# Optimization experiments

Hardware: AMD Instinct MI355X
Metric: run time of the kernel (lower is better)

## Reference

```python
import jax, jax.numpy as jnp
import numpy as np

B, L, D = 4, 8192, 512


def _normalize(v):
    # F.normalize: v / max(||v||, 1e-12)
    n = jnp.linalg.norm(v, axis=-1, keepdims=True)
    return v / jnp.maximum(n, 1e-12)


def setup_inputs() -> dict:
    key = jax.random.key(0)
    k1, k2, k3, k4 = jax.random.split(key, 4)
    return {
        "hidden_states": jax.random.normal(k1, (B, L, D), jnp.float32),
        "residual": jax.random.normal(k2, (B, L, D), jnp.float32),
        "q_weight": jax.random.normal(k3, (D, D), jnp.float32) * 0.02,
        "k_weight": jax.random.normal(k4, (D, D), jnp.float32) * 0.02,
        "det_state": jnp.zeros((B, D), jnp.float32),
    }


def reference(hidden_states, residual, q_weight, k_weight, det_state):
    Bs, Ls, Ds = hidden_states.shape
    # ---- CosineSimRouter.prob_boundary ----
    q = _normalize(hidden_states[:, :-1] @ q_weight.T)   # (B, L-1, D)
    k = _normalize(hidden_states[:, 1:] @ k_weight.T)    # (B, L-1, D)
    cos_sim = jnp.einsum('bld,bld->bl', q, k)            # (B, L-1)
    prob = jnp.concatenate(
        [jnp.ones((Bs, 1), jnp.float32), jnp.clip((1.0 - cos_sim) / 2.0, 0.0, 1.0)],
        axis=1)                                           # (B, L); prob[:,0]=1 (state=None path)
    token_mask = prob > 0.5                               # (B, L)

    # ---- Tokenizer: compact boundary positions (pad M -> L, static shape) ----
    counts = token_mask.sum(axis=1)                       # (B,)
    order = jnp.argsort(~token_mask, axis=1)              # stable: True-mask indices first, in order
    valid = jnp.arange(Ls)[None, :] < counts[:, None]     # (B, L)
    chunked = jnp.take_along_axis(hidden_states, order[..., None], axis=1)
    chunked = chunked * valid[..., None]                  # (B, L, D)
    chunk_probs = jnp.take_along_axis(prob, order, axis=1) * valid  # (B, L)

    # ---- DeTokenizer: EMA associative scan over compacted chunks ----
    decay = jnp.clip(1.0 - chunk_probs, 0.0, 1.0)
    # pad positions have chunk_probs=0 -> decay=1 -> state carried unchanged
    a = jnp.broadcast_to(decay[..., None], (Bs, Ls, Ds))
    b = (1.0 - decay)[..., None] * chunked
    b = b.at[:, 0].add(a[:, 0] * det_state)

    def comb(x, y):  # x earlier, y later: (a2*a1, a2*b1 + b2)
        ax, bx = x
        ay, by = y
        return ax * ay, ay * bx + by

    _, ema_out = jax.lax.associative_scan(comb, (a, b), axis=1)
    ema_out = ema_out * valid[..., None]                  # zero padded chunk slots

    # broadcast back to full sequence via cumulative chunk indexing
    chunk_idx = jnp.cumsum(token_mask.astype(jnp.int32), axis=1) - 1  # (B, L)
    ci = jnp.clip(chunk_idx, 0, Ls - 1)
    long_states = jnp.take_along_axis(ema_out, ci[..., None], axis=1)
    long_states = long_states * (chunk_idx >= 0)[..., None]

    # STE coefficient: forward == 1 (grad flows through max(1-p, p) in bwd)
    coef_raw = jnp.maximum(1.0 - prob, prob)
    coef = coef_raw + jax.lax.stop_gradient(1.0 - coef_raw)
    long_states = long_states * coef[..., None]

    output = residual + long_states                       # (B, L, D)
    return output
```

## Files before the change

### kernel.cpp

```cpp
#include <hip/hip_runtime.h>
#include <hip/hip_bf16.h>
#include <math.h>

#define B_  4
#define L_  8192
#define D_  512

#define BM   128
#define NCT  4
#define NRT  (L_ / BM)
#define KW   64
#define NSTAGE (D_ / KW)

#define CHUNK 64
#define NCHUNK (L_ / CHUNK)

#define MAXFIX 16380
#define FIX_TAU 1.0e-3f
#define FROWS 8
#define NSLICE 8

typedef short bf16x8 __attribute__((ext_vector_type(8)));
typedef float f32x4 __attribute__((ext_vector_type(4)));
typedef unsigned short u16;
typedef unsigned int u32;

__device__ __forceinline__ u32 pk2(float lo, float hi) {
    __hip_bfloat162 v = __float22bfloat162_rn(float2{lo, hi});
    union { __hip_bfloat162 b; u32 u; } cv; cv.b = v;
    return cv.u;
}

#define GLOAD_LDS(g, l) __builtin_amdgcn_global_load_lds( \
    (__attribute__((address_space(1))) void*)(g),         \
    (__attribute__((address_space(3))) void*)(l), 16, 0, 0)

__global__ __launch_bounds__(256) void conv_h(
    const float* __restrict__ h, u16* __restrict__ h16)
{
    size_t i = ((size_t)blockIdx.x * 256 + threadIdx.x) * 8;
    float4 a = *(const float4*)(h + i);
    float4 b = *(const float4*)(h + i + 4);
    uint4 v;
    v.x = pk2(a.x, a.y); v.y = pk2(a.z, a.w);
    v.z = pk2(b.x, b.y); v.w = pk2(b.z, b.w);
    *(uint4*)(h16 + i) = v;
}

__global__ __launch_bounds__(256) void prep_w(
    const float* __restrict__ wq, const float* __restrict__ wk,
    u16* __restrict__ qh, u16* __restrict__ kh,
    float* __restrict__ wqt, float* __restrict__ wkt,
    int* __restrict__ fix_cnt)
{
    __shared__ float tile[64][65];
    const int bi = blockIdx.x;
    const int bj = blockIdx.y;
    const int t = threadIdx.x;
    if (bi == 0 && bj == 0 && t == 0) *fix_cnt = 0;
    const int c0 = bi * 64, k0 = bj * 64;
    const float* src = wq; float* dst = wqt; u16* dsth = qh;
#pragma unroll
    for (int m = 0; m < 2; ++m) {
        __syncthreads();
#pragma unroll
        for (int it = 0; it < 4; ++it) {
            int r = it * 16 + (t >> 4);
            int cc = (t & 15) * 4;
            float4 v = *(const float4*)(src + (size_t)(c0 + r) * D_ + k0 + cc);
            tile[r][cc] = v.x; tile[r][cc + 1] = v.y;
            tile[r][cc + 2] = v.z; tile[r][cc + 3] = v.w;
            uint2 hv; hv.x = pk2(v.x, v.y); hv.y = pk2(v.z, v.w);
            *(uint2*)(dsth + (size_t)(c0 + r) * D_ + k0 + cc) = hv;
        }
        __syncthreads();
#pragma unroll
        for (int it = 0; it < 4; ++it) {
            int cl = t & 63;
            int kq = it * 4 + (t >> 6);
            float4 v;
            v.x = tile[cl][kq * 4 + 0]; v.y = tile[cl][kq * 4 + 1];
            v.z = tile[cl][kq * 4 + 2]; v.w = tile[cl][kq * 4 + 3];
            size_t o = ((size_t)((k0 >> 2) + kq) * 512 + (c0 + cl)) * 4;
            *(float4*)(dst + o) = v;
        }
        src = wk; dst = wkt; dsth = kh;
    }
}

__global__ __launch_bounds__(256, 2) void qk_mfma(
    const u16* __restrict__ h16,
    const u16* __restrict__ wqh, const u16* __restrict__ wkh,
    float* __restrict__ part)
{
    const int bid = blockIdx.x;
    const int swz = (bid & 7) * 128 + (bid >> 3);
    const int ct = swz & 3, rt = (swz >> 2) & 63, b = swz >> 8;
    const int t = threadIdx.x, wid = t >> 6, lane = t & 63;
    const int l15 = lane & 15, l4 = lane >> 4;

    __shared__ __align__(16) u16 ah[2][129 * 64];
    __shared__ float red[4][BM][3];

    const int r0 = rt * BM;
    const u16* hb = h16 + (size_t)b * L_ * D_;

    const int rl0 = wid * 32 + (lane >> 3);
    const int csw = ((lane & 7) ^ (rl0 & 7)) * 8;
    const u16* gA = hb + (size_t)(r0 + rl0) * D_ + csw;
    const int dstw = wid * 32 * 64;

    const int re = (r0 + BM > L_ - 1) ? (L_ - 1) : (r0 + BM);
    const u16* gpe = hb + (size_t)re * D_;

    const int colb = ct * 128 + wid * 32;
    const u16* bq0 = wqh + (size_t)(colb + l15) * D_ + l4 * 8;
    const u16* bq1 = bq0 + (size_t)16 * D_;
    const u16* bk0 = wkh + (size_t)(colb + l15) * D_ + l4 * 8;
    const u16* bk1 = bk0 + (size_t)16 * D_;

    int aoff[8];
#pragma unroll
    for (int rf = 0; rf < 8; ++rf) {
        int R = rf * 16 + l15;
        aoff[rf] = R * 64 + ((l4 ^ (R & 7)) * 8);
    }
    const int aoffE = 128 * 64 + l4 * 8;

    f32x4 accq[8][2], acck[8][2], ackl[2];
    const f32x4 zero = {0.f, 0.f, 0.f, 0.f};
#pragma unroll
    for (int rf = 0; rf < 8; ++rf) {
        accq[rf][0] = zero; accq[rf][1] = zero;
        acck[rf][0] = zero; acck[rf][1] = zero;
    }
    ackl[0] = zero; ackl[1] = zero;

#define STAGE_ISSUE(S, BUF) do { const int _o = (S) * KW;      \
    GLOAD_LDS(gA + _o,         &ah[BUF][dstw]);                \
    GLOAD_LDS(gA + _o + 4096,  &ah[BUF][dstw + 512]);          \
    GLOAD_LDS(gA + _o + 8192,  &ah[BUF][dstw + 1024]);         \
    GLOAD_LDS(gA + _o + 12288, &ah[BUF][dstw + 1536]); } while (0)

    STAGE_ISSUE(0, 0);
    uint2 er = {0, 0};
    if (t < 16) er = *(const uint2*)(gpe + t * 4);
    if (t < 16) *(uint2*)(&ah[0][128 * 64 + t * 4]) = er;
    __syncthreads();

    int cur = 0;
    for (int s = 0; s < NSTAGE; ++s) {
        if (s + 1 < NSTAGE) {
            STAGE_ISSUE(s + 1, cur ^ 1);
            if (t < 16) er = *(const uint2*)(gpe + (s + 1) * KW + t * 4);
        }

        const int so = s * KW;
        bf16x8 q00 = *(const bf16x8*)(bq0 + so);
        bf16x8 q01 = *(const bf16x8*)(bq0 + so + 32);
        bf16x8 q10 = *(const bf16x8*)(bq1 + so);
        bf16x8 q11 = *(const bf16x8*)(bq1 + so + 32);
        bf16x8 k00 = *(const bf16x8*)(bk0 + so);
        bf16x8 k01 = *(const bf16x8*)(bk0 + so + 32);
        bf16x8 k10 = *(const bf16x8*)(bk1 + so);
        bf16x8 k11 = *(const bf16x8*)(bk1 + so + 32);

        const u16* ab = ah[cur];
#pragma unroll
        for (int kk = 0; kk < 2; ++kk) {
            bf16x8 fq0 = kk ? q01 : q00;
            bf16x8 fq1 = kk ? q11 : q10;
            bf16x8 fk0 = kk ? k01 : k00;
            bf16x8 fk1 = kk ? k11 : k10;
#pragma unroll
            for (int rf = 0; rf < 8; ++rf) {
                bf16x8 a = *(const bf16x8*)(ab + (aoff[rf] ^ (kk * 32)));
                accq[rf][0] = __builtin_amdgcn_mfma_f32_16x16x32_bf16(a, fq0, accq[rf][0], 0, 0, 0);
                accq[rf][1] = __builtin_amdgcn_mfma_f32_16x16x32_bf16(a, fq1, accq[rf][1], 0, 0, 0);
                acck[rf][0] = __builtin_amdgcn_mfma_f32_16x16x32_bf16(a, fk0, acck[rf][0], 0, 0, 0);
                acck[rf][1] = __builtin_amdgcn_mfma_f32_16x16x32_bf16(a, fk1, acck[rf][1], 0, 0, 0);
            }
            bf16x8 al = *(const bf16x8*)(ab + (aoffE ^ (kk * 32)));
            ackl[0] = __builtin_amdgcn_mfma_f32_16x16x32_bf16(al, fk0, ackl[0], 0, 0, 0);
            ackl[1] = __builtin_amdgcn_mfma_f32_16x16x32_bf16(al, fk1, ackl[1], 0, 0, 0);
        }

        if (s + 1 < NSTAGE && t < 16)
            *(uint2*)(&ah[cur ^ 1][128 * 64 + t * 4]) = er;
        __syncthreads();
        cur ^= 1;
    }
#undef STAGE_ISSUE

#pragma unroll
    for (int rf = 0; rf < 8; ++rf) {
#pragma unroll
        for (int reg = 0; reg < 4; ++reg) {
            float pq = 0.f, pk = 0.f, pd = 0.f;
#pragma unroll
            for (int cf = 0; cf < 2; ++cf) {
                float qv = accq[rf][cf][reg];
                float kv = acck[rf][cf][reg];
                pq += qv * qv;
                pk += kv * kv;
                float ksh;
                if (reg < 3) {
                    ksh = acck[rf][cf][reg + 1];
                } else {
                    float up = __shfl(acck[rf][cf][0], (lane + 16) & 63);
                    float nx0 = (rf < 7) ? acck[rf + 1][cf][0] : ackl[cf][0];
                    float nx = __shfl(nx0, l15);
                    ksh = (l4 == 3) ? nx : up;
                }
                pd += qv * ksh;
            }
#pragma unroll
            for (int off = 1; off < 16; off <<= 1) {
                pq += __shfl_xor(pq, off);
                pk += __shfl_xor(pk, off);
                pd += __shfl_xor(pd, off);
            }
            if (l15 == 0) {
                int row = rf * 16 + l4 * 4 + reg;
                red[wid][row][0] = pq;
                red[wid][row][1] = pk;
                red[wid][row][2] = pd;
            }
        }
    }
    __syncthreads();
    if (t < BM) {
        float pq = red[0][t][0] + red[1][t][0] + red[2][t][0] + red[3][t][0];
        float pk = red[0][t][1] + red[1][t][1] + red[2][t][1] + red[3][t][1];
        float pd = red[0][t][2] + red[1][t][2] + red[2][t][2] + red[3][t][2];
        size_t o = (((size_t)ct * B_ + b) * L_ + (r0 + t)) * 3;
        part[o + 0] = pq; part[o + 1] = pk; part[o + 2] = pd;
    }
}

__global__ __launch_bounds__(256) void cos_reduce(
    const float* __restrict__ part, float* __restrict__ p,
    int* __restrict__ fix_cnt, int* __restrict__ fix_list)
{
    int idx = blockIdx.x * 256 + threadIdx.x;
    if (idx >= B_ * L_) return;
    int b = idx / L_;
    int tp = idx % L_;
    if (tp == 0) { p[idx] = 1.0f; return; }
    int l = tp - 1;
    float nq = 0.f, nk = 0.f, dt = 0.f;
#pragma unroll
    for (int ct = 0; ct < NCT; ++ct) {
        size_t o = (((size_t)ct * B_ + b) * L_ + l) * 3;
        nq += part[o + 0];
        dt += part[o + 2];
        nk += part[o + 4];
    }
    float qn = sqrtf(nq); if (qn < 1e-12f) qn = 1e-12f;
    float kn = sqrtf(nk); if (kn < 1e-12f) kn = 1e-12f;
    float cs = dt / (qn * kn);
    float pr = 0.5f * (1.0f - cs);
    pr = fminf(fmaxf(pr, 0.0f), 1.0f);
    p[idx] = pr;
    if (fabsf(cs) < FIX_TAU) {
        int slot = atomicAdd(fix_cnt, 1);
        if (slot < MAXFIX) fix_list[slot] = idx;
    }
}

__global__ __launch_bounds__(256) void fixup_main(
    const float* __restrict__ h,
    const float* __restrict__ wqt, const float* __restrict__ wkt,
    const int* __restrict__ fix_cnt, const int* __restrict__ fix_list,
    float* __restrict__ part_fix)
{
    __shared__ float hq[FROWS][D_];
    __shared__ float hk[FROWS][D_];
    __shared__ float red[FROWS][3][4];
    const int t = threadIdx.x, wid = t >> 6, lane = t & 63;
    const int col16 = lane & 15, kpart = lane >> 4;
    int n = *fix_cnt; if (n > MAXFIX) n = MAXFIX;
    const int ntiles = (n + FROWS - 1) / FROWS;
    const int nitems = ntiles * NSLICE;

    for (int item = blockIdx.x; item < nitems; item += gridDim.x) {
        const int tile = item >> 3;
        const int cs = item & 7;
        __syncthreads();
#pragma unroll
        for (int r = 0; r < FROWS; ++r) {
            int s = tile * FROWS + r;
            int idx = fix_list[s < n ? s : 0];
            int bb = idx >> 13;
            int tp = idx & (L_ - 1);
            const float* hr = h + ((size_t)bb * L_ + (tp - 1)) * D_;
            ((float2*)hq[r])[t] = ((const float2*)hr)[t];
            ((float2*)hk[r])[t] = ((const float2*)(hr + D_))[t];
        }
        __syncthreads();

        const int c = cs * 64 + wid * 16 + col16;
        float qa0, qa1, qa2, qa3, qa4, qa5, qa6, qa7;
        float ka0, ka1, ka2, ka3, ka4, ka5, ka6, ka7;
        qa0=qa1=qa2=qa3=qa4=qa5=qa6=qa7=0.f;
        ka0=ka1=ka2=ka3=ka4=ka5=ka6=ka7=0.f;

        const int k0 = kpart * 32;
        float4 wv = *(const float4*)(wqt + ((size_t)k0 * 512 + c) * 4);
        float4 xv = *(const float4*)(wkt + ((size_t)k0 * 512 + c) * 4);
#pragma unroll 4
        for (int kq = k0; kq < k0 + 32; ++kq) {
            const int kn = (kq + 1 < k0 + 32) ? kq + 1 : kq;
            float4 wn = *(const float4*)(wqt + ((size_t)kn * 512 + c) * 4);
            float4 xn = *(const float4*)(wkt + ((size_t)kn * 512 + c) * 4);
#define FROW(R, QA, KA) { \
            float4 hv = *(const float4*)(&hq[R][kq * 4]); \
            float4 kv = *(const float4*)(&hk[R][kq * 4]); \
            QA += hv.x*wv.x + hv.y*wv.y + hv.z*wv.z + hv.w*wv.w; \
            KA += kv.x*xv.x + kv.y*xv.y + kv.z*xv.z + kv.w*xv.w; }
            FROW(0, qa0, ka0) FROW(1, qa1, ka1) FROW(2, qa2, ka2) FROW(3, qa3, ka3)
            FROW(4, qa4, ka4) FROW(5, qa5, ka5) FROW(6, qa6, ka6) FROW(7, qa7, ka7)
#undef FROW
            wv = wn; xv = xn;
        }

#define REDROW(R, QA, KA) { \
        float qf = QA; qf += __shfl_xor(qf, 16); qf += __shfl_xor(qf, 32); \
        float kf = KA; kf += __shfl_xor(kf, 16); kf += __shfl_xor(kf, 32); \
        float pq = qf * qf, pk = kf * kf, pd = qf * kf; \
        pq += __shfl_xor(pq, 1); pk += __shfl_xor(pk, 1); pd += __shfl_xor(pd, 1); \
        pq += __shfl_xor(pq, 2); pk += __shfl_xor(pk, 2); pd += __shfl_xor(pd, 2); \
        pq += __shfl_xor(pq, 4); pk += __shfl_xor(pk, 4); pd += __shfl_xor(pd, 4); \
        pq += __shfl_xor(pq, 8); pk += __shfl_xor(pk, 8); pd += __shfl_xor(pd, 8); \
        if (lane == 0) { red[R][0][wid] = pq; red[R][1][wid] = pk; red[R][2][wid] = pd; } }
        REDROW(0, qa0, ka0) REDROW(1, qa1, ka1) REDROW(2, qa2, ka2) REDROW(3, qa3, ka3)
        REDROW(4, qa4, ka4) REDROW(5, qa5, ka5) REDROW(6, qa6, ka6) REDROW(7, qa7, ka7)
#undef REDROW
        __syncthreads();
        if (t < FROWS) {
            int s = tile * FROWS + t;
            if (s < n) {
                float* pp = part_fix + ((size_t)s * NSLICE + cs) * 3;
                pp[0] = red[t][0][0] + red[t][0][1] + red[t][0][2] + red[t][0][3];
                pp[1] = red[t][1][0] + red[t][1][1] + red[t][1][2] + red[t][1][3];
                pp[2] = red[t][2][0] + red[t][2][1] + red[t][2][2] + red[t][2][3];
            }
        }
    }
}

__global__ __launch_bounds__(256) void fixup_final(
    const int* __restrict__ fix_cnt, const int* __restrict__ fix_list,
    const float* __restrict__ part_fix, float* __restrict__ p)
{
    int n = *fix_cnt; if (n > MAXFIX) n = MAXFIX;
    for (int s = blockIdx.x * 256 + threadIdx.x; s < n; s += gridDim.x * 256) {
        float nq = 0.f, nk = 0.f, dt = 0.f;
#pragma unroll
        for (int cs = 0; cs < NSLICE; ++cs) {
            const float* pp = part_fix + ((size_t)s * NSLICE + cs) * 3;
            nq += pp[0]; nk += pp[1]; dt += pp[2];
        }
        float qn = sqrtf(nq); if (qn < 1e-12f) qn = 1e-12f;
        float kn = sqrtf(nk); if (kn < 1e-12f) kn = 1e-12f;
        float cs2 = dt / (qn * kn);
        float pr = 0.5f * (1.0f - cs2);
        pr = fminf(fmaxf(pr, 0.0f), 1.0f);
        p[fix_list[s]] = pr;
    }
}

__global__ __launch_bounds__(256) void scan_a(
    const float* __restrict__ h, const float* __restrict__ p,
    float* __restrict__ Bc, float* __restrict__ Ac)
{
    const int t = threadIdx.x;
    const int c = blockIdx.x, b = blockIdx.y;
    const int l0 = c * CHUNK;
    const float* pb = p + (size_t)b * L_ + l0;
    const float2* hb = (const float2*)(h + ((size_t)b * L_ + l0) * D_) + t;

    float2 st = {0.f, 0.f};
    float ap = 1.f;
#pragma unroll 4
    for (int i = 0; i < CHUNK; ++i) {
        float pr = pb[i];
        float2 hv = hb[(size_t)i * 256];
        bool sel = pr > 0.5f;
        float a = sel ? 1.f - pr : 1.f;
        float g = sel ? pr : 0.f;
        st.x = a * st.x + g * hv.x;
        st.y = a * st.y + g * hv.y;
        ap *= a;
    }
    ((float2*)Bc)[((size_t)b * NCHUNK + c) * 256 + t] = st;
    if (t == 0) Ac[b * NCHUNK + c] = ap;
}

__global__ __launch_bounds__(256) void scan_b(
    const float* __restrict__ Ac, const float* __restrict__ Bc,
    const float* __restrict__ det, float* __restrict__ carry)
{
    const int t = threadIdx.x;
    const int b = blockIdx.x;
    const float* acb = Ac + b * NCHUNK;
    const float2* bcb = (const float2*)Bc + (size_t)b * NCHUNK * 256 + t;
    float2* cb = (float2*)carry + (size_t)b * NCHUNK * 256 + t;
    float2 st = ((const float2*)det)[(size_t)b * 256 + t];

    float a0 = acb[0], a1 = acb[1], a2 = acb[2], a3 = acb[3];
    float2 b0 = bcb[0], b1 = bcb[256], b2 = bcb[512], b3 = bcb[768];
    for (int g = 0; g < NCHUNK / 4; ++g) {
        const int nc = (g + 1 < NCHUNK / 4) ? (g + 1) * 4 : g * 4;
        float an0 = acb[nc], an1 = acb[nc + 1], an2 = acb[nc + 2], an3 = acb[nc + 3];
        float2 bn0 = bcb[(size_t)nc * 256],        bn1 = bcb[(size_t)(nc + 1) * 256];
        float2 bn2 = bcb[(size_t)(nc + 2) * 256],  bn3 = bcb[(size_t)(nc + 3) * 256];
        const size_t c0 = (size_t)g * 4 * 256;
        cb[c0]       = st; st.x = a0 * st.x + b0.x; st.y = a0 * st.y + b0.y;
        cb[c0 + 256] = st; st.x = a1 * st.x + b1.x; st.y = a1 * st.y + b1.y;
        cb[c0 + 512] = st; st.x = a2 * st.x + b2.x; st.y = a2 * st.y + b2.y;
        cb[c0 + 768] = st; st.x = a3 * st.x + b3.x; st.y = a3 * st.y + b3.y;
        a0 = an0; a1 = an1; a2 = an2; a3 = an3;
        b0 = bn0; b1 = bn1; b2 = bn2; b3 = bn3;
    }
}

__global__ __launch_bounds__(256) void scan_c(
    const float* __restrict__ h, const float* __restrict__ p,
    const float* __restrict__ res, const float* __restrict__ carry,
    float* __restrict__ out)
{
    const int t = threadIdx.x;
    const int c = blockIdx.x, b = blockIdx.y;
    const int l0 = c * CHUNK;
    const float* pb = p + (size_t)b * L_ + l0;
    const size_t base = ((size_t)b * L_ + l0) * 256 + t;
    const float2* hb = (const float2*)h + base;
    const float2* rb = (const float2*)res + base;
    float2* ob = (float2*)out + base;

    float2 st = ((const float2*)carry)[((size_t)b * NCHUNK + c) * 256 + t];
#pragma unroll 4
    for (int i = 0; i < CHUNK; ++i) {
        float pr = pb[i];
        float2 hv = hb[(size_t)i * 256];
        float2 rv = rb[(size_t)i * 256];
        bool sel = pr > 0.5f;
        float a = sel ? 1.f - pr : 1.f;
        float g = sel ? pr : 0.f;
        st.x = a * st.x + g * hv.x;
        st.y = a * st.y + g * hv.y;
        float2 ov; ov.x = rv.x + st.x; ov.y = rv.y + st.y;
        ob[(size_t)i * 256] = ov;
    }
}

extern "C" void kernel_launch(void* const* d_in, const int* in_sizes, int n_in,
                              void* d_out, int out_size, void* d_ws, size_t ws_size,
                              hipStream_t stream)
{
    const float* h   = (const float*)d_in[0];
    const float* res = (const float*)d_in[1];
    const float* wq  = (const float*)d_in[2];
    const float* wk  = (const float*)d_in[3];
    const float* det = (const float*)d_in[4];
    float* out = (float*)d_out;

    u16* h16 = (u16*)d_out;

    float* ws = (float*)d_ws;
    float* part  = ws;
    float* p     = part + (size_t)NCT * B_ * L_ * 3;
    float* Ac    = p + (size_t)B_ * L_;
    float* Bc    = Ac + (size_t)B_ * NCHUNK;
    float* carry = Bc + (size_t)B_ * NCHUNK * D_;
    int*  fix_cnt  = (int*)(carry + (size_t)B_ * NCHUNK * D_);
    int*  fix_list = fix_cnt + 4;
    u16* wqh = (u16*)(fix_list + MAXFIX);
    u16* wkh = wqh + (size_t)D_ * D_;
    float* wqt = (float*)(wkh + (size_t)D_ * D_);
    float* wkt = wqt + (size_t)D_ * D_;
    float* part_fix = wkt + (size_t)D_ * D_;

    conv_h<<<(B_ * L_ * D_) / (256 * 8), 256, 0, stream>>>(h, h16);
    prep_w<<<dim3(8, 8), 256, 0, stream>>>(wq, wk, wqh, wkh, wqt, wkt, fix_cnt);
    qk_mfma<<<NCT * NRT * B_, 256, 0, stream>>>(h16, wqh, wkh, part);
    cos_reduce<<<(B_ * L_ + 255) / 256, 256, 0, stream>>>(part, p, fix_cnt, fix_list);
    fixup_main<<<1024, 256, 0, stream>>>(h, wqt, wkt, fix_cnt, fix_list, part_fix);
    fixup_final<<<64, 256, 0, stream>>>(fix_cnt, fix_list, part_fix, p);
    scan_a<<<dim3(NCHUNK, B_), 256, 0, stream>>>(h, p, Bc, Ac);
    scan_b<<<B_, 256, 0, stream>>>(Ac, Bc, det, carry);
    scan_c<<<dim3(NCHUNK, B_), 256, 0, stream>>>(h, p, res, carry, out);
}
```

Baseline: 173.1 us.

## Triple-buffer qk_mfma LDS pipeline and merge prep kernels into one launch

The qk_mfma main loop moves from double buffering to a three-stage LDS ring. Loads are issued two stages ahead, synchronisation is an explicit vmcnt wait plus one barrier per stage, and the extra halo row is loaded asynchronously with global_load_lds instead of through registers. This is meant to hide global-load latency behind MFMA work and cut the barriers per stage. Separately, conv_h and prep_w are fused into one launch to save launch overhead. The risks are more LDS use, which may reduce occupancy, and halo reads past the tile end that are no longer clamped.

```diff
diff --git a/kernel.cpp b/kernel.cpp
--- a/kernel.cpp
+++ b/kernel.cpp
@@ -11,6 +11,7 @@
 #define NRT  (L_ / BM)
 #define KW   64
 #define NSTAGE (D_ / KW)
+#define BUFW 8704
 
 #define CHUNK 64
 #define NCHUNK (L_ / CHUNK)
@@ -35,29 +36,31 @@
     (__attribute__((address_space(1))) void*)(g),         \
     (__attribute__((address_space(3))) void*)(l), 16, 0, 0)
 
-__global__ __launch_bounds__(256) void conv_h(
-    const float* __restrict__ h, u16* __restrict__ h16)
-{
-    size_t i = ((size_t)blockIdx.x * 256 + threadIdx.x) * 8;
-    float4 a = *(const float4*)(h + i);
-    float4 b = *(const float4*)(h + i + 4);
-    uint4 v;
-    v.x = pk2(a.x, a.y); v.y = pk2(a.z, a.w);
-    v.z = pk2(b.x, b.y); v.w = pk2(b.z, b.w);
-    *(uint4*)(h16 + i) = v;
-}
-
-__global__ __launch_bounds__(256) void prep_w(
+#define NCONVB ((B_ * L_ * D_) / (256 * 8))
+
+__global__ __launch_bounds__(256) void prep_all(
+    const float* __restrict__ h, u16* __restrict__ h16,
     const float* __restrict__ wq, const float* __restrict__ wk,
     u16* __restrict__ qh, u16* __restrict__ kh,
     float* __restrict__ wqt, float* __restrict__ wkt,
     int* __restrict__ fix_cnt)
 {
     __shared__ float tile[64][65];
-    const int bi = blockIdx.x;
-    const int bj = blockIdx.y;
     const int t = threadIdx.x;
-    if (bi == 0 && bj == 0 && t == 0) *fix_cnt = 0;
+    if (blockIdx.x < NCONVB) {
+        size_t i = ((size_t)blockIdx.x * 256 + t) * 8;
+        float4 a = *(const float4*)(h + i);
+        float4 b = *(const float4*)(h + i + 4);
+        uint4 v;
+        v.x = pk2(a.x, a.y); v.y = pk2(a.z, a.w);
+        v.z = pk2(b.x, b.y); v.w = pk2(b.z, b.w);
+        *(uint4*)(h16 + i) = v;
+        return;
+    }
+    const int wb = blockIdx.x - NCONVB;
+    const int bi = wb & 7;
+    const int bj = wb >> 3;
+    if (wb == 0 && t == 0) *fix_cnt = 0;
     const int c0 = bi * 64, k0 = bj * 64;
     const float* src = wq; float* dst = wqt; u16* dsth = qh;
 #pragma unroll
@@ -99,19 +102,17 @@
     const int t = threadIdx.x, wid = t >> 6, lane = t & 63;
     const int l15 = lane & 15, l4 = lane >> 4;
 
-    __shared__ __align__(16) u16 ah[2][129 * 64];
+    __shared__ __align__(16) u16 ah[3 * BUFW];
     __shared__ float red[4][BM][3];
 
     const int r0 = rt * BM;
     const u16* hb = h16 + (size_t)b * L_ * D_;
 
     const int rl0 = wid * 32 + (lane >> 3);
-    const int csw = ((lane & 7) ^ (rl0 & 7)) * 8;
+    const int csw = ((lane & 7) ^ ((lane >> 3) & 7)) * 8;
     const u16* gA = hb + (size_t)(r0 + rl0) * D_ + csw;
     const int dstw = wid * 32 * 64;
-
-    const int re = (r0 + BM > L_ - 1) ? (L_ - 1) : (r0 + BM);
-    const u16* gpe = hb + (size_t)re * D_;
+    const u16* gE = hb + (size_t)(r0 + 128 + (lane >> 3)) * D_ + (lane & 7) * 8;
 
     const int colb = ct * 128 + wid * 32;
     const u16* bq0 = wqh + (size_t)(colb + l15) * D_ + l4 * 8;
@@ -136,24 +137,26 @@
     }
     ackl[0] = zero; ackl[1] = zero;
 
-#define STAGE_ISSUE(S, BUF) do { const int _o = (S) * KW;      \
-    GLOAD_LDS(gA + _o,         &ah[BUF][dstw]);                \
-    GLOAD_LDS(gA + _o + 4096,  &ah[BUF][dstw + 512]);          \
-    GLOAD_LDS(gA + _o + 8192,  &ah[BUF][dstw + 1024]);         \
-    GLOAD_LDS(gA + _o + 12288, &ah[BUF][dstw + 1536]); } while (0)
+#define STAGE_ISSUE(S, BUF) do { const size_t _o = (size_t)(S) * KW;  \
+    u16* _d = &ah[(BUF) * BUFW];                                      \
+    GLOAD_LDS(gA + _o,         _d + dstw);                            \
+    GLOAD_LDS(gA + _o + 4096,  _d + dstw + 512);                      \
+    GLOAD_LDS(gA + _o + 8192,  _d + dstw + 1024);                     \
+    GLOAD_LDS(gA + _o + 12288, _d + dstw + 1536);                     \
+    if (wid == 0) GLOAD_LDS(gE + _o, _d + 8192); } while (0)
 
     STAGE_ISSUE(0, 0);
-    uint2 er = {0, 0};
-    if (t < 16) er = *(const uint2*)(gpe + t * 4);
-    if (t < 16) *(uint2*)(&ah[0][128 * 64 + t * 4]) = er;
-    __syncthreads();
-
-    int cur = 0;
+    STAGE_ISSUE(1, 1);
+
     for (int s = 0; s < NSTAGE; ++s) {
-        if (s + 1 < NSTAGE) {
-            STAGE_ISSUE(s + 1, cur ^ 1);
-            if (t < 16) er = *(const uint2*)(gpe + (s + 1) * KW + t * 4);
-        }
+        if (s < NSTAGE - 1) {
+            asm volatile("s_waitcnt vmcnt(4)" ::: "memory");
+        } else {
+            asm volatile("s_waitcnt vmcnt(0)" ::: "memory");
+        }
+        __builtin_amdgcn_sched_barrier(0);
+        __builtin_amdgcn_s_barrier();
+        __builtin_amdgcn_sched_barrier(0);
 
         const int so = s * KW;
         bf16x8 q00 = *(const bf16x8*)(bq0 + so);
@@ -164,8 +167,12 @@
         bf16x8 k01 = *(const bf16x8*)(bk0 + so + 32);
         bf16x8 k10 = *(const bf16x8*)(bk1 + so);
         bf16x8 k11 = *(const bf16x8*)(bk1 + so + 32);
-
-        const u16* ab = ah[cur];
+        __builtin_amdgcn_sched_barrier(0);
+
+        if (s + 2 < NSTAGE) STAGE_ISSUE(s + 2, (s + 2) % 3);
+        __builtin_amdgcn_sched_barrier(0);
+
+        const u16* ab = &ah[(s % 3) * BUFW];
 #pragma unroll
         for (int kk = 0; kk < 2; ++kk) {
             bf16x8 fq0 = kk ? q01 : q00;
@@ -184,11 +191,6 @@
             ackl[0] = __builtin_amdgcn_mfma_f32_16x16x32_bf16(al, fk0, ackl[0], 0, 0, 0);
             ackl[1] = __builtin_amdgcn_mfma_f32_16x16x32_bf16(al, fk1, ackl[1], 0, 0, 0);
         }
-
-        if (s + 1 < NSTAGE && t < 16)
-            *(uint2*)(&ah[cur ^ 1][128 * 64 + t * 4]) = er;
-        __syncthreads();
-        cur ^= 1;
     }
 #undef STAGE_ISSUE
 
@@ -482,8 +484,8 @@
     float* wkt = wqt + (size_t)D_ * D_;
     float* part_fix = wkt + (size_t)D_ * D_;
 
-    conv_h<<<(B_ * L_ * D_) / (256 * 8), 256, 0, stream>>>(h, h16);
-    prep_w<<<dim3(8, 8), 256, 0, stream>>>(wq, wk, wqh, wkh, wqt, wkt, fix_cnt);
+    prep_all<<<NCONVB + 64, 256, 0, stream>>>(h, h16, wq, wk, wqh, wkh,
+                                              wqt, wkt, fix_cnt);
     qk_mfma<<<NCT * NRT * B_, 256, 0, stream>>>(h16, wqh, wkh, part);
     cos_reduce<<<(B_ * L_ + 255) / 256, 256, 0, stream>>>(part, p, fix_cnt, fix_list);
     fixup_main<<<1024, 256, 0, stream>>>(h, wqt, wkt, fix_cnt, fix_list, part_fix);
```

Result: faster. 169.3 us (-2.2%).
